# Optimization experiments

Hardware: AMD Instinct MI355X
Metric: run time of the kernel (lower is better)

Reference implementation:

```python
import jax, jax.numpy as jnp
import numpy as np

N_E = 8192
E_DIM = 256
LATENT = 768
OUT_DIM = 768
DECAY = 0.99
EPS = 1e-05
DEAD_THRESH = 0.05
RESET_CS = DEAD_THRESH * 1.2  # reset_cluster_size
RATIO = (8 * 2048) / N_E      # total_codes / n_e with world_size=1


def l2norm(t):
    return t / jnp.linalg.norm(t, axis=-1, keepdims=True)


def setup_inputs() -> dict:
    key = jax.random.key(0)
    ks = jax.random.split(key, 6)
    x = jax.random.normal(ks[0], (8, 2048, LATENT), dtype=jnp.float32)
    # project_in / project_out Linear params (torch Linear: y = x @ W.T + b)
    W_in = jax.random.normal(ks[1], (E_DIM, LATENT), dtype=jnp.float32) * (1.0 / np.sqrt(LATENT))
    b_in = jnp.zeros((E_DIM,), dtype=jnp.float32)
    W_out = jax.random.normal(ks[2], (OUT_DIM, E_DIM), dtype=jnp.float32) * (1.0 / np.sqrt(E_DIM))
    b_out = jnp.zeros((OUT_DIM,), dtype=jnp.float32)
    embed = jax.random.uniform(ks[3], (N_E, E_DIM), dtype=jnp.float32,
                               minval=-1.0 / N_E, maxval=1.0 / N_E)
    embed = l2norm(embed)
    embed_avg = embed
    cluster_size = jnp.ones((N_E,), dtype=jnp.float32) * RATIO  # after init_quantizer
    return {"x": x, "W_in": W_in, "b_in": b_in, "W_out": W_out, "b_out": b_out,
            "embed": embed, "embed_avg": embed_avg, "cluster_size": cluster_size}


def reference(x, W_in, b_in, W_out, b_out, embed, embed_avg, cluster_size):
    sg = jax.lax.stop_gradient
    x_proj = jnp.einsum('btl,el->bte', x, W_in) + b_in        # [B,T,e_dim]
    xf = x_proj.reshape(-1, E_DIM)                            # [n, e_dim]
    xn = l2norm(xf)
    embed_d = sg(embed)
    d = jnp.einsum('nd,cd->nc', xn, embed_d)                  # [n, n_e] similarity
    embed_ind = jnp.argmin(d, axis=1)                         # (faithful: argmin of dot)
    onehot = jax.nn.one_hot(embed_ind, N_E, dtype=jnp.float32)
    z_q = jnp.einsum('nc,cd->nd', onehot, embed_d)            # training path
    bins = onehot.sum(axis=0)                                 # [n_e]
    cluster_new = cluster_size * DECAY + bins * (1.0 - DECAY)
    embed_sum = jnp.einsum('nd,nc->cd', xn, onehot)
    embed_avg_new = embed_avg * DECAY + embed_sum * (1.0 - DECAY)
    # laplace smoothing * total
    total = cluster_new.sum()
    cs = (cluster_new + EPS) / (total + N_E * EPS) * total
    embed_norm = embed_avg_new / cs[:, None]
    # entropy losses on scaled distances
    p = jax.nn.softmax(d * 10.0, axis=-1)                     # [n, n_e]
    ap = p.mean(axis=0)
    entropy_to_max = -(ap * jnp.log(ap)).sum()
    entropy_to_min = (-(p * jnp.log(p)).sum(axis=-1)).mean()
    diversity_loss = -entropy_to_max
    commit_loss = jnp.mean((sg(z_q) - xn) ** 2)
    loss = 1.0 * commit_loss + 1.0 * diversity_loss
    # straight-through estimator
    z_q_st = xn + sg(z_q - xn)
    z_q_out = z_q_st.reshape(x_proj.shape)
    z_q_out = jnp.einsum('bte,oe->bto', z_q_out, W_out) + b_out
    # expire dead codes: replace with first k samples (masked, jit-friendly)
    expired = cluster_new < DEAD_THRESH * RATIO
    n = xn.shape[0]
    idx = jnp.clip(jnp.cumsum(expired.astype(jnp.int32)) - 1, 0, None) % n
    sampled = sg(xn)[idx]                                     # [n_e, e_dim]
    embed_final = jnp.where(expired[:, None], sampled, embed_norm)
    embed_avg_final = jnp.where(expired[:, None], sampled * (RESET_CS * RATIO), embed_avg_new)
    cluster_final = jnp.where(expired, RESET_CS * RATIO, cluster_new)
    return (z_q_out, embed_ind, loss, embed_final, embed_avg_final, cluster_final,
            entropy_to_min, commit_loss)
```

## Files before the change

### kernel.cpp

```cpp
#include <hip/hip_runtime.h>
#include <hip/hip_bf16.h>

typedef unsigned long long u64;
typedef __bf16 bf16_t;
typedef __attribute__((ext_vector_type(8))) __bf16 bf16x8;
typedef __attribute__((ext_vector_type(4))) __bf16 bf16x4;
typedef __attribute__((ext_vector_type(4))) float f32x4;

#define NROWS 16384
#define KLAT  768
#define EDIM  256
#define NE    8192
#define ODIM  768

#define OFF_ZQ   0
#define OFF_IND  12582912
#define OFF_LOSS 12599296
#define OFF_EMB  12599297
#define OFF_EAVG 14696449
#define OFF_CSF  16793601
#define OFF_EMIN 16801793
#define OFF_CMT  16801794

#define W_XN    0u
#define W_ESUM  16777216u
#define W_RMIN  25165824u
#define W_RZ    25296896u
#define W_RS1   25362432u
#define W_INVZ  25427968u
#define W_INDW  25493504u
#define W_BINS  25559040u
#define W_CN    25591808u
#define W_CSM   25624576u
#define W_IDXS  25657344u
#define W_AP    25690112u
#define W_SCAL  25722880u
#define W_END   25722896u

#define CANDCAP 16
#define PROWS   2048
#define PM      128
#define PN      128
#define PK      32

typedef __attribute__((address_space(3))) unsigned char lds_u8;
typedef __attribute__((address_space(1))) const unsigned char glb_u8;
static __device__ __forceinline__ void gload16(const void* g, void* l)
{
  __builtin_amdgcn_global_load_lds((glb_u8*)g, (lds_u8*)l, 16, 0, 0);
}

__global__ __launch_bounds__(256) void zero_out_kernel(float* __restrict__ out, int n)
{
  int i = blockIdx.x * 256 + threadIdx.x;
  if (i < n) out[i] = 0.0f;
}

__global__ __launch_bounds__(256) void gemm_in_kernel(
    const float* __restrict__ A, const float* __restrict__ B,
    const float* __restrict__ bias, float* __restrict__ C)
{
  __shared__ float As[16][64];
  __shared__ float Bs[16][64];
  const int tid = threadIdx.x;
  const int tx = tid & 15, ty = tid >> 4;
  const int bm = blockIdx.x << 6, bn = blockIdx.y << 6;
  const int lr = tid >> 2, lk = (tid & 3) << 2;
  const size_t aoff = (size_t)(bm + lr) * KLAT;
  const size_t boff = (size_t)(bn + lr) * KLAT;
  float acc[4][4] = {};
  for (int k0 = 0; k0 < KLAT; k0 += 16) {
    __syncthreads();
    float4 av = *(const float4*)(A + aoff + k0 + lk);
    float4 bv = *(const float4*)(B + boff + k0 + lk);
    As[lk + 0][lr] = av.x; As[lk + 1][lr] = av.y; As[lk + 2][lr] = av.z; As[lk + 3][lr] = av.w;
    Bs[lk + 0][lr] = bv.x; Bs[lk + 1][lr] = bv.y; Bs[lk + 2][lr] = bv.z; Bs[lk + 3][lr] = bv.w;
    __syncthreads();
#pragma unroll
    for (int kk = 0; kk < 16; ++kk) {
      float4 a4 = *(const float4*)&As[kk][ty << 2];
      float4 b4 = *(const float4*)&Bs[kk][tx << 2];
      float ar[4] = {a4.x, a4.y, a4.z, a4.w};
      float br[4] = {b4.x, b4.y, b4.z, b4.w};
#pragma unroll
      for (int i = 0; i < 4; ++i)
#pragma unroll
        for (int j = 0; j < 4; ++j)
          acc[i][j] = fmaf(ar[i], br[j], acc[i][j]);
    }
  }
  float4 b4 = *(const float4*)(bias + bn + (tx << 2));
  float bb[4] = {b4.x, b4.y, b4.z, b4.w};
#pragma unroll
  for (int i = 0; i < 4; ++i) {
    const size_t row = (size_t)(bm + (ty << 2) + i);
    float4 o = make_float4(acc[i][0] + bb[0], acc[i][1] + bb[1],
                           acc[i][2] + bb[2], acc[i][3] + bb[3]);
    *(float4*)(C + row * EDIM + bn + (tx << 2)) = o;
  }
}

__global__ __launch_bounds__(256) void gemm_out_kernel(
    const float* __restrict__ A, const float* __restrict__ B,
    const float* __restrict__ bias, const int* __restrict__ gather,
    float* __restrict__ C)
{
  __shared__ float As[16][64];
  __shared__ float Bs[16][64];
  const int tid = threadIdx.x;
  const int tx = tid & 15, ty = tid >> 4;
  const int bm = blockIdx.x << 6, bn = blockIdx.y << 6;
  const int lr = tid >> 2, lk = (tid & 3) << 2;
  const size_t arow = (size_t)(gather[bm + lr] & (NE - 1));
  const size_t aoff = arow * EDIM;
  const size_t boff = (size_t)(bn + lr) * EDIM;
  float acc[4][4] = {};
  for (int k0 = 0; k0 < EDIM; k0 += 16) {
    __syncthreads();
    float4 av = *(const float4*)(A + aoff + k0 + lk);
    float4 bv = *(const float4*)(B + boff + k0 + lk);
    As[lk + 0][lr] = av.x; As[lk + 1][lr] = av.y; As[lk + 2][lr] = av.z; As[lk + 3][lr] = av.w;
    Bs[lk + 0][lr] = bv.x; Bs[lk + 1][lr] = bv.y; Bs[lk + 2][lr] = bv.z; Bs[lk + 3][lr] = bv.w;
    __syncthreads();
#pragma unroll
    for (int kk = 0; kk < 16; ++kk) {
      float4 a4 = *(const float4*)&As[kk][ty << 2];
      float4 b4 = *(const float4*)&Bs[kk][tx << 2];
      float ar[4] = {a4.x, a4.y, a4.z, a4.w};
      float br[4] = {b4.x, b4.y, b4.z, b4.w};
#pragma unroll
      for (int i = 0; i < 4; ++i)
#pragma unroll
        for (int j = 0; j < 4; ++j)
          acc[i][j] = fmaf(ar[i], br[j], acc[i][j]);
    }
  }
  float4 b4 = *(const float4*)(bias + bn + (tx << 2));
  float bb[4] = {b4.x, b4.y, b4.z, b4.w};
#pragma unroll
  for (int i = 0; i < 4; ++i) {
    const size_t row = (size_t)(bm + (ty << 2) + i);
    float4 o = make_float4(acc[i][0] + bb[0], acc[i][1] + bb[1],
                           acc[i][2] + bb[2], acc[i][3] + bb[3]);
    *(float4*)(C + row * ODIM + bn + (tx << 2)) = o;
  }
}

__global__ __launch_bounds__(256) void l2norm_split_kernel(
    float* __restrict__ xnf, bf16_t* __restrict__ xh, bf16_t* __restrict__ xl)
{
  __shared__ float sb[4];
  const int r = blockIdx.x, t = threadIdx.x;
  const size_t o = (size_t)r * EDIM + t;
  float v = xnf[o];
  float s = v * v;
#pragma unroll
  for (int off = 32; off >= 1; off >>= 1) s += __shfl_xor(s, off);
  if ((t & 63) == 0) sb[t >> 6] = s;
  __syncthreads();
  float tot = sb[0] + sb[1] + sb[2] + sb[3];
  float nv = v / sqrtf(tot);
  xnf[o] = nv;
  bf16_t h = (bf16_t)nv;
  xh[o] = h;
  xl[o] = (bf16_t)(nv - (float)h);
}

__global__ __launch_bounds__(256) void embed_split_kernel(
    const float* __restrict__ embed, bf16_t* __restrict__ eh, bf16_t* __restrict__ el)
{
  const int i = (blockIdx.x * 256 + threadIdx.x) << 2;
  float4 v = *(const float4*)(embed + i);
  bf16_t h0 = (bf16_t)v.x, h1 = (bf16_t)v.y, h2 = (bf16_t)v.z, h3 = (bf16_t)v.w;
  bf16x4 hv = {h0, h1, h2, h3};
  bf16x4 lv = {(bf16_t)(v.x - (float)h0), (bf16_t)(v.y - (float)h1),
               (bf16_t)(v.z - (float)h2), (bf16_t)(v.w - (float)h3)};
  *(bf16x4*)(eh + i) = hv;
  *(bf16x4*)(el + i) = lv;
}

__global__ __launch_bounds__(256) void phase1_mfma_kernel(
    const bf16_t* __restrict__ xh, const bf16_t* __restrict__ xl,
    const bf16_t* __restrict__ eh, const bf16_t* __restrict__ el,
    const int rowbase,
    u64* __restrict__ rowmin, float* __restrict__ rowZ, float* __restrict__ rowS1,
    bf16_t* __restrict__ P)
{
  __shared__ bf16_t Ab[PM * 64];
  __shared__ bf16_t Bb[PN * 64];
  const int tid  = threadIdx.x;
  const int lane = tid & 63;
  const int wave = tid >> 6;
  const int wm = wave >> 1, wn = wave & 1;
  const int brow = blockIdx.x * PM;
  const int bcol = blockIdx.y * PN;

  const int srow8 = lane >> 3;
  const int chunk = (lane & 7) ^ srow8;
  const bf16_t* gpa = (chunk & 4) ? xl : xh;
  const bf16_t* gpb = (chunk & 4) ? el : eh;
  const int within = (chunk & 3) << 3;
  const int acall0 = wave << 5;

  const bf16_t* ga0 = gpa + (size_t)(rowbase + brow + acall0 + srow8) * EDIM + within;
  const bf16_t* gb0 = gpb + (size_t)(bcol + acall0 + srow8) * EDIM + within;

  f32x4 acc[4][4] = {};

  for (int k0 = 0; k0 < EDIM; k0 += PK) {
    __syncthreads();
#pragma unroll
    for (int c = 0; c < 4; ++c) {
      const int rr = acall0 + (c << 3);
      gload16(ga0 + (size_t)(c << 3) * EDIM + k0, &Ab[rr * 64]);
      gload16(gb0 + (size_t)(c << 3) * EDIM + k0, &Bb[rr * 64]);
    }
    __syncthreads();

    const int swz = lane & 7;
    const int sh  = (lane >> 4) ^ swz;
    const int sl  = sh ^ 4;
    const int ar0 = (wm << 6) + (lane & 15);
    const int br0 = (wn << 6) + (lane & 15);
    bf16x8 bhf[4], blf[4];
#pragma unroll
    for (int n = 0; n < 4; ++n) {
      const int r = br0 + (n << 4);
      bhf[n] = *(const bf16x8*)&Bb[r * 64 + (sh << 3)];
      blf[n] = *(const bf16x8*)&Bb[r * 64 + (sl << 3)];
    }
#pragma unroll
    for (int m = 0; m < 4; ++m) {
      const int r = ar0 + (m << 4);
      bf16x8 ahf = *(const bf16x8*)&Ab[r * 64 + (sh << 3)];
      bf16x8 alf = *(const bf16x8*)&Ab[r * 64 + (sl << 3)];
#pragma unroll
      for (int n = 0; n < 4; ++n) {
        acc[m][n] = __builtin_amdgcn_mfma_f32_16x16x32_bf16(ahf, bhf[n], acc[m][n], 0, 0, 0);
        acc[m][n] = __builtin_amdgcn_mfma_f32_16x16x32_bf16(ahf, blf[n], acc[m][n], 0, 0, 0);
        acc[m][n] = __builtin_amdgcn_mfma_f32_16x16x32_bf16(alf, bhf[n], acc[m][n], 0, 0, 0);
      }
    }
  }

  const int colg  = bcol + (wn << 6) + (lane & 15);
  const int pbase = bcol + (wn << 6) + ((lane & 15) << 2);
  const int rl0   = brow + (wm << 6) + ((lane >> 4) << 2);
#pragma unroll
  for (int m = 0; m < 4; ++m) {
#pragma unroll
    for (int q = 0; q < 4; ++q) {
      const int rl = rl0 + (m << 4) + q;
      float Z = 0.f, S1 = 0.f;
      u64 mk = ~0ull;
      bf16_t evv[4];
#pragma unroll
      for (int n = 0; n < 4; ++n) {
        float d = acc[m][n][q];
        float l = 10.f * d;
        float e = __expf(l);
        Z += e; S1 += l * e;
        evv[n] = (bf16_t)e;
        u64 key = ((u64)__float_as_uint(d + 2.0f) << 32) | (unsigned)(colg + (n << 4));
        if (key < mk) mk = key;
      }
      bf16x4 pv = {evv[0], evv[1], evv[2], evv[3]};
      *(bf16x4*)(P + (size_t)rl * NE + pbase) = pv;
#pragma unroll
      for (int off = 1; off < 16; off <<= 1) {
        u64 ok = __shfl_xor(mk, off);
        if (ok < mk) mk = ok;
        Z  += __shfl_xor(Z, off);
        S1 += __shfl_xor(S1, off);
      }
      if ((lane & 15) == 0) {
        const int rg = rowbase + rl;
        atomicMin(rowmin + rg, mk);
        atomicAdd(rowZ + rg, Z);
        atomicAdd(rowS1 + rg, S1);
      }
    }
  }
}

__global__ __launch_bounds__(256) void colreduce_kernel(
    const bf16_t* __restrict__ P, const float* __restrict__ rowZ,
    const u64* __restrict__ rowmin, const int rowbase,
    float* __restrict__ ap, int* __restrict__ ccnt, int* __restrict__ clist)
{
  __shared__ float izs[64], ths[64];
  const int t = threadIdx.x;
  const int pc0 = blockIdx.x * 1024 + (t << 2);
  const int r0 = blockIdx.y * 64;
  if (t < 64) {
    const int rg = rowbase + r0 + t;
    izs[t] = 1.0f / rowZ[rg];
    float dmin = __uint_as_float((unsigned)(rowmin[rg] >> 32)) - 2.0f;
    ths[t] = __expf(10.f * (dmin + 3e-4f));
  }
  __syncthreads();
  const int Bbase = pc0 & ~63;
  const int sub   = (pc0 & 63) >> 2;
  float s0 = 0.f, s1 = 0.f, s2 = 0.f, s3 = 0.f;
  for (int r = 0; r < 64; ++r) {
    bf16x4 p4 = *(const bf16x4*)(P + (size_t)(r0 + r) * NE + pc0);
    float p0 = (float)p4[0], p1 = (float)p4[1], p2 = (float)p4[2], p3 = (float)p4[3];
    float iz = izs[r], th = ths[r];
    s0 = fmaf(p0, iz, s0); s1 = fmaf(p1, iz, s1);
    s2 = fmaf(p2, iz, s2); s3 = fmaf(p3, iz, s3);
    float pm = fminf(fminf(p0, p1), fminf(p2, p3));
    if (pm <= th) {
      const int rg = rowbase + r0 + r;
      float pvv[4] = {p0, p1, p2, p3};
      for (int n = 0; n < 4; ++n)
        if (pvv[n] <= th) {
          int pos = atomicAdd(ccnt + rg, 1);
          if (pos < CANDCAP) clist[(rg << 4) + pos] = Bbase + (n << 4) + sub;
        }
    }
  }
  atomicAdd(ap + pc0 + 0, s0); atomicAdd(ap + pc0 + 1, s1);
  atomicAdd(ap + pc0 + 2, s2); atomicAdd(ap + pc0 + 3, s3);
}

__global__ __launch_bounds__(256) void rowent_kernel(
    const float* __restrict__ rowZ, const float* __restrict__ rowS1,
    float* __restrict__ scal)
{
  __shared__ float sb[4];
  const int r = blockIdx.x * 256 + threadIdx.x;
  const int t = threadIdx.x;
  float Z = rowZ[r], S1 = rowS1[r];
  float ent = logf(Z) - S1 / Z;
#pragma unroll
  for (int off = 32; off >= 1; off >>= 1) ent += __shfl_xor(ent, off);
  if ((t & 63) == 0) sb[t >> 6] = ent;
  __syncthreads();
  if (t == 0) atomicAdd(scal + 1, sb[0] + sb[1] + sb[2] + sb[3]);
}

__global__ __launch_bounds__(256) void repair_kernel(
    const float* __restrict__ xnf, const float* __restrict__ embed,
    const u64* __restrict__ rowmin, const int* __restrict__ ccnt,
    const int* __restrict__ clist, int* __restrict__ indw,
    float* __restrict__ bins, int* __restrict__ binsI, float* __restrict__ out)
{
  const int t = threadIdx.x;
  const int row = blockIdx.x * 64 + (t >> 2);
  const int sub = t & 3;
  const int base = ((int)(unsigned)(rowmin[row] & 0xFFFFFFFFull)) & (NE - 1);
  int cnt = ccnt[row];
  if (cnt > CANDCAP) cnt = CANDCAP;
  float bestD = 1e30f;
  int bestI = NE;
  const float* xr = xnf + (size_t)row * EDIM + (sub << 6);
  for (int j = -1; j < cnt; ++j) {
    const int c = (j < 0) ? base : (clist[(row << 4) + j] & (NE - 1));
    const float* er = embed + (size_t)c * EDIM + (sub << 6);
    float s = 0.f;
#pragma unroll
    for (int k = 0; k < 64; k += 4) {
      float4 a = *(const float4*)(xr + k);
      float4 b = *(const float4*)(er + k);
      s = fmaf(a.x, b.x, s); s = fmaf(a.y, b.y, s);
      s = fmaf(a.z, b.z, s); s = fmaf(a.w, b.w, s);
    }
    s += __shfl_xor(s, 1);
    s += __shfl_xor(s, 2);
    if (s < bestD || (s == bestD && c < bestI)) { bestD = s; bestI = c; }
  }
  if (sub == 0) {
    indw[row] = bestI;
    out[OFF_IND + row] = (float)bestI;
    atomicAdd(bins + bestI, 1.0f);
    atomicAdd(binsI + bestI, 1);
  }
}

__global__ __launch_bounds__(256) void sortprep_kernel(
    const int* __restrict__ binsI, int* __restrict__ offs, int* __restrict__ cursor)
{
  __shared__ int ssum[256];
  const int t = threadIdx.x;
  const int base = t * 32;
  int loc[32];
  int cnt = 0;
#pragma unroll
  for (int j = 0; j < 32; ++j) { loc[j] = cnt; cnt += binsI[base + j]; }
  ssum[t] = cnt;
  __syncthreads();
  for (int off = 1; off < 256; off <<= 1) {
    int v = (t >= off) ? ssum[t - off] : 0;
    __syncthreads();
    ssum[t] += v;
    __syncthreads();
  }
  int run = (t > 0) ? ssum[t - 1] : 0;
#pragma unroll
  for (int j = 0; j < 32; ++j) {
    offs[base + j]   = run + loc[j];
    cursor[base + j] = run + loc[j];
  }
}

__global__ __launch_bounds__(256) void rowsort_kernel(
    const int* __restrict__ indw, int* __restrict__ cursor, int* __restrict__ sorted)
{
  const int r = blockIdx.x * 256 + threadIdx.x;
  const int ind = indw[r] & (NE - 1);
  int pos = atomicAdd(cursor + ind, 1);
  sorted[pos & (NROWS - 1)] = r;
}

__global__ __launch_bounds__(256) void esum_commit_kernel(
    const int* __restrict__ offs, const int* __restrict__ binsI,
    const int* __restrict__ sorted, const float* __restrict__ xnf,
    const float* __restrict__ embed, float* __restrict__ esum,
    float* __restrict__ scal)
{
  __shared__ float sb[4];
  const int c = blockIdx.x, t = threadIdx.x;
  const float ev = embed[(size_t)c * EDIM + t];
  const int start = offs[c];
  const int cnt = binsI[c];
  float s = 0.f, cm = 0.f;
  for (int j = 0; j < cnt; ++j) {
    const int r = sorted[(start + j) & (NROWS - 1)];
    float xv = xnf[(size_t)r * EDIM + t];
    s += xv;
    float df = ev - xv;
    cm = fmaf(df, df, cm);
  }
  esum[(size_t)c * EDIM + t] = s;
#pragma unroll
  for (int off = 32; off >= 1; off >>= 1) cm += __shfl_xor(cm, off);
  if ((t & 63) == 0) sb[t >> 6] = cm;
  __syncthreads();
  if (t == 0) atomicAdd(scal + 2, sb[0] + sb[1] + sb[2] + sb[3]);
}

__global__ __launch_bounds__(256) void scalars_kernel(
    const float* __restrict__ ap, const float* __restrict__ scal, float* __restrict__ out)
{
  __shared__ float sb[4];
  const int t = threadIdx.x;
  float h = 0.f;
  for (int c = t; c < NE; c += 256) {
    float apv = ap[c] * (1.0f / NROWS);
    h -= apv * logf(apv);
  }
#pragma unroll
  for (int off = 32; off >= 1; off >>= 1) h += __shfl_xor(h, off);
  if ((t & 63) == 0) sb[t >> 6] = h;
  __syncthreads();
  if (t == 0) {
    float Hmax = sb[0] + sb[1] + sb[2] + sb[3];
    float commit = scal[2] * (1.0f / ((float)NROWS * (float)EDIM));
    float emin = scal[1] * (1.0f / (float)NROWS);
    out[OFF_LOSS] = commit - Hmax;
    out[OFF_EMIN] = emin;
    out[OFF_CMT]  = commit;
  }
}

__global__ __launch_bounds__(256) void cluster_kernel(
    const float* __restrict__ cs_in, const float* __restrict__ bins,
    float* __restrict__ cn, float* __restrict__ scal)
{
  __shared__ float sb[4];
  const int c = blockIdx.x * 256 + threadIdx.x;
  const int t = threadIdx.x;
  float v = cs_in[c] * 0.99f + bins[c] * 0.01f;
  cn[c] = v;
  float s = v;
#pragma unroll
  for (int off = 32; off >= 1; off >>= 1) s += __shfl_xor(s, off);
  if ((t & 63) == 0) sb[t >> 6] = s;
  __syncthreads();
  if (t == 0) atomicAdd(scal + 0, sb[0] + sb[1] + sb[2] + sb[3]);
}

__global__ __launch_bounds__(256) void scan_kernel(
    const float* __restrict__ cn, const float* __restrict__ scal,
    int* __restrict__ idxs, float* __restrict__ csm, float* __restrict__ out)
{
  __shared__ int ssum[256];
  const int t = threadIdx.x;
  const int base = t * 32;
  int cnt = 0;
  for (int j = 0; j < 32; ++j) cnt += (cn[base + j] < 0.1f) ? 1 : 0;
  ssum[t] = cnt;
  __syncthreads();
  for (int off = 1; off < 256; off <<= 1) {
    int v = (t >= off) ? ssum[t - off] : 0;
    __syncthreads();
    ssum[t] += v;
    __syncthreads();
  }
  int run = (t > 0) ? ssum[t - 1] : 0;
  const float total = scal[0];
  const float dscale = total / (total + (float)NE * 1e-5f);
  for (int j = 0; j < 32; ++j) {
    float v = cn[base + j];
    bool ex = v < 0.1f;
    run += ex ? 1 : 0;
    int idx = run - 1; if (idx < 0) idx = 0;
    idx &= (NROWS - 1);
    idxs[base + j] = idx;
    csm[base + j] = (v + 1e-5f) * dscale;
    out[OFF_CSF + base + j] = ex ? 0.12f : v;
  }
}

__global__ __launch_bounds__(256) void embed_out_kernel(
    const float* __restrict__ cn, const float* __restrict__ csm,
    const int* __restrict__ idxs, const float* __restrict__ xn,
    const float* __restrict__ embed_avg, const float* __restrict__ esum,
    float* __restrict__ out)
{
  const int c = blockIdx.x, t = threadIdx.x;
  float oe, oa;
  if (cn[c] < 0.1f) {
    float s = xn[(size_t)(idxs[c] & (NROWS - 1)) * EDIM + t];
    oe = s; oa = s * 0.12f;
  } else {
    float an = embed_avg[(size_t)c * EDIM + t] * 0.99f
             + esum[(size_t)c * EDIM + t] * 0.01f;
    oa = an; oe = an / csm[c];
  }
  out[OFF_EMB  + (size_t)c * EDIM + t] = oe;
  out[OFF_EAVG + (size_t)c * EDIM + t] = oa;
}

extern "C" void kernel_launch(void* const* d_in, const int* in_sizes, int n_in,
                              void* d_out, int out_size, void* d_ws, size_t ws_size,
                              hipStream_t stream)
{
  const float* x         = (const float*)d_in[0];
  const float* W_in      = (const float*)d_in[1];
  const float* b_in      = (const float*)d_in[2];
  const float* W_out     = (const float*)d_in[3];
  const float* b_out     = (const float*)d_in[4];
  const float* embed     = (const float*)d_in[5];
  const float* embed_avg = (const float*)d_in[6];
  const float* cs_in     = (const float*)d_in[7];
  float* out = (float*)d_out;
  char* ws = (char*)d_ws;

  if (ws_size < (size_t)W_END) {
    zero_out_kernel<<<(out_size + 255) / 256, 256, 0, stream>>>(out, out_size);
    return;
  }

  bf16_t* xh = (bf16_t*)(ws + W_XN);
  bf16_t* xl = (bf16_t*)(ws + W_XN + 8388608u);
  bf16_t* eh = (bf16_t*)(ws + W_ESUM);
  bf16_t* el = (bf16_t*)(ws + W_ESUM + 4194304u);
  float* esum  = (float*)(ws + W_ESUM);
  u64*   rowmin= (u64*)  (ws + W_RMIN);
  int*   offs  = (int*)  (ws + W_RMIN);
  int*   cursor= offs + NE;
  float* rowZ  = (float*)(ws + W_RZ);
  float* rowS1 = (float*)(ws + W_RS1);
  int*   binsI = (int*)  (ws + W_INVZ);
  int*   indw  = (int*)  (ws + W_INDW);
  float* bins  = (float*)(ws + W_BINS);
  float* cn    = (float*)(ws + W_CN);
  float* csm   = (float*)(ws + W_CSM);
  int*   idxs  = (int*)  (ws + W_IDXS);
  float* ap    = (float*)(ws + W_AP);
  float* scal  = (float*)(ws + W_SCAL);

  float*  xnf    = out + OFF_ZQ;
  bf16_t* Pbuf   = (bf16_t*)(out + OFF_ZQ + 4194304);
  int*    ccnt   = (int*)(out + OFF_EMB);
  int*    clist  = ccnt + NROWS;
  int*    sorted = clist + NROWS * CANDCAP;

  hipMemsetAsync(ws + W_RMIN, 0xFF, W_RZ - W_RMIN, stream);
  hipMemsetAsync(ws + W_RZ,   0,    W_END - W_RZ,  stream);
  hipMemsetAsync(ccnt, 0, NROWS * sizeof(int), stream);

  gemm_in_kernel<<<dim3(NROWS / 64, EDIM / 64), 256, 0, stream>>>(
      x, W_in, b_in, xnf);
  l2norm_split_kernel<<<NROWS, 256, 0, stream>>>(xnf, xh, xl);
  embed_split_kernel<<<(NE * EDIM / 4) / 256, 256, 0, stream>>>(embed, eh, el);
  for (int p = 0; p < NROWS / PROWS; ++p) {
    const int rowbase = p * PROWS;
    phase1_mfma_kernel<<<dim3(PROWS / PM, NE / PN), 256, 0, stream>>>(
        xh, xl, eh, el, rowbase, rowmin, rowZ, rowS1, Pbuf);
    colreduce_kernel<<<dim3(NE / 1024, PROWS / 64), 256, 0, stream>>>(
        Pbuf, rowZ, rowmin, rowbase, ap, ccnt, clist);
  }
  rowent_kernel<<<NROWS / 256, 256, 0, stream>>>(rowZ, rowS1, scal);
  repair_kernel<<<NROWS / 64, 256, 0, stream>>>(
      xnf, embed, rowmin, ccnt, clist, indw, bins, binsI, out);
  sortprep_kernel<<<1, 256, 0, stream>>>(binsI, offs, cursor);
  rowsort_kernel<<<NROWS / 256, 256, 0, stream>>>(indw, cursor, sorted);
  esum_commit_kernel<<<NE, 256, 0, stream>>>(
      offs, binsI, sorted, xnf, embed, esum, scal);
  cluster_kernel<<<NE / 256, 256, 0, stream>>>(cs_in, bins, cn, scal);
  scan_kernel<<<1, 256, 0, stream>>>(cn, scal, idxs, csm, out);
  scalars_kernel<<<1, 256, 0, stream>>>(ap, scal, out);
  embed_out_kernel<<<NE, 256, 0, stream>>>(cn, csm, idxs, xnf, embed_avg, esum, out);
  gemm_out_kernel<<<dim3(NROWS / 64, ODIM / 64), 256, 0, stream>>>(
      embed, W_out, b_out, indw, out + OFF_ZQ);
}
```

Baseline: 1.168 ms.

## Move output projection to split-bf16 MFMA, pad input GEMM LDS, cheapen argmin reduction

Replaces the fp32 SIMT output GEMM with an MFMA kernel. It gathers codebook rows from the bf16 hi/lo split of embed and splits W_out into hi/lo the same way, then uses three MFMAs per tile to keep near-fp32 accuracy. It also pads the input GEMM's shared-memory tiles to reduce LDS bank conflicts. In the phase1 epilogue, the 64-bit key shuffle reduction becomes a float min shuffle, so only lanes holding the minimum issue the atomicMin. Workspace is reshuffled so esum and the W_out split share the old xh/xl region, which relies on those buffers being dead by then.

```diff
diff --git a/kernel.cpp b/kernel.cpp
--- a/kernel.cpp
+++ b/kernel.cpp
@@ -60,8 +60,8 @@
     const float* __restrict__ A, const float* __restrict__ B,
     const float* __restrict__ bias, float* __restrict__ C)
 {
-  __shared__ float As[16][64];
-  __shared__ float Bs[16][64];
+  __shared__ float As[16][68];
+  __shared__ float Bs[16][68];
   const int tid = threadIdx.x;
   const int tx = tid & 15, ty = tid >> 4;
   const int bm = blockIdx.x << 6, bn = blockIdx.y << 6;
@@ -100,52 +100,6 @@
   }
 }
 
-__global__ __launch_bounds__(256) void gemm_out_kernel(
-    const float* __restrict__ A, const float* __restrict__ B,
-    const float* __restrict__ bias, const int* __restrict__ gather,
-    float* __restrict__ C)
-{
-  __shared__ float As[16][64];
-  __shared__ float Bs[16][64];
-  const int tid = threadIdx.x;
-  const int tx = tid & 15, ty = tid >> 4;
-  const int bm = blockIdx.x << 6, bn = blockIdx.y << 6;
-  const int lr = tid >> 2, lk = (tid & 3) << 2;
-  const size_t arow = (size_t)(gather[bm + lr] & (NE - 1));
-  const size_t aoff = arow * EDIM;
-  const size_t boff = (size_t)(bn + lr) * EDIM;
-  float acc[4][4] = {};
-  for (int k0 = 0; k0 < EDIM; k0 += 16) {
-    __syncthreads();
-    float4 av = *(const float4*)(A + aoff + k0 + lk);
-    float4 bv = *(const float4*)(B + boff + k0 + lk);
-    As[lk + 0][lr] = av.x; As[lk + 1][lr] = av.y; As[lk + 2][lr] = av.z; As[lk + 3][lr] = av.w;
-    Bs[lk + 0][lr] = bv.x; Bs[lk + 1][lr] = bv.y; Bs[lk + 2][lr] = bv.z; Bs[lk + 3][lr] = bv.w;
-    __syncthreads();
-#pragma unroll
-    for (int kk = 0; kk < 16; ++kk) {
-      float4 a4 = *(const float4*)&As[kk][ty << 2];
-      float4 b4 = *(const float4*)&Bs[kk][tx << 2];
-      float ar[4] = {a4.x, a4.y, a4.z, a4.w};
-      float br[4] = {b4.x, b4.y, b4.z, b4.w};
-#pragma unroll
-      for (int i = 0; i < 4; ++i)
-#pragma unroll
-        for (int j = 0; j < 4; ++j)
-          acc[i][j] = fmaf(ar[i], br[j], acc[i][j]);
-    }
-  }
-  float4 b4 = *(const float4*)(bias + bn + (tx << 2));
-  float bb[4] = {b4.x, b4.y, b4.z, b4.w};
-#pragma unroll
-  for (int i = 0; i < 4; ++i) {
-    const size_t row = (size_t)(bm + (ty << 2) + i);
-    float4 o = make_float4(acc[i][0] + bb[0], acc[i][1] + bb[1],
-                           acc[i][2] + bb[2], acc[i][3] + bb[3]);
-    *(float4*)(C + row * ODIM + bn + (tx << 2)) = o;
-  }
-}
-
 __global__ __launch_bounds__(256) void l2norm_split_kernel(
     float* __restrict__ xnf, bf16_t* __restrict__ xh, bf16_t* __restrict__ xl)
 {
@@ -166,17 +120,17 @@
   xl[o] = (bf16_t)(nv - (float)h);
 }
 
-__global__ __launch_bounds__(256) void embed_split_kernel(
-    const float* __restrict__ embed, bf16_t* __restrict__ eh, bf16_t* __restrict__ el)
+__global__ __launch_bounds__(256) void split_kernel(
+    const float* __restrict__ src, bf16_t* __restrict__ hi, bf16_t* __restrict__ lo)
 {
   const int i = (blockIdx.x * 256 + threadIdx.x) << 2;
-  float4 v = *(const float4*)(embed + i);
+  float4 v = *(const float4*)(src + i);
   bf16_t h0 = (bf16_t)v.x, h1 = (bf16_t)v.y, h2 = (bf16_t)v.z, h3 = (bf16_t)v.w;
   bf16x4 hv = {h0, h1, h2, h3};
   bf16x4 lv = {(bf16_t)(v.x - (float)h0), (bf16_t)(v.y - (float)h1),
                (bf16_t)(v.z - (float)h2), (bf16_t)(v.w - (float)h3)};
-  *(bf16x4*)(eh + i) = hv;
-  *(bf16x4*)(el + i) = lv;
+  *(bf16x4*)(hi + i) = hv;
+  *(bf16x4*)(lo + i) = lv;
 }
 
 __global__ __launch_bounds__(256) void phase1_mfma_kernel(
@@ -252,7 +206,8 @@
     for (int q = 0; q < 4; ++q) {
       const int rl = rl0 + (m << 4) + q;
       float Z = 0.f, S1 = 0.f;
-      u64 mk = ~0ull;
+      float dloc = 1e30f;
+      int nbest = 0;
       bf16_t evv[4];
 #pragma unroll
       for (int n = 0; n < 4; ++n) {
@@ -261,21 +216,24 @@
         float e = __expf(l);
         Z += e; S1 += l * e;
         evv[n] = (bf16_t)e;
-        u64 key = ((u64)__float_as_uint(d + 2.0f) << 32) | (unsigned)(colg + (n << 4));
-        if (key < mk) mk = key;
+        if (d < dloc) { dloc = d; nbest = n; }
       }
       bf16x4 pv = {evv[0], evv[1], evv[2], evv[3]};
       *(bf16x4*)(P + (size_t)rl * NE + pbase) = pv;
+      float dmin = dloc;
 #pragma unroll
       for (int off = 1; off < 16; off <<= 1) {
-        u64 ok = __shfl_xor(mk, off);
-        if (ok < mk) mk = ok;
+        dmin = fminf(dmin, __shfl_xor(dmin, off));
         Z  += __shfl_xor(Z, off);
         S1 += __shfl_xor(S1, off);
       }
+      const int rg = rowbase + rl;
+      if (dloc == dmin) {
+        u64 key = ((u64)__float_as_uint(dloc + 2.0f) << 32)
+                | (unsigned)(colg + (nbest << 4));
+        atomicMin(rowmin + rg, key);
+      }
       if ((lane & 15) == 0) {
-        const int rg = rowbase + rl;
-        atomicMin(rowmin + rg, mk);
         atomicAdd(rowZ + rg, Z);
         atomicAdd(rowS1 + rg, S1);
       }
@@ -532,6 +490,91 @@
   out[OFF_EAVG + (size_t)c * EDIM + t] = oa;
 }
 
+__global__ __launch_bounds__(256) void gemm_out_mfma_kernel(
+    const bf16_t* __restrict__ eh, const bf16_t* __restrict__ el,
+    const bf16_t* __restrict__ wh, const bf16_t* __restrict__ wl,
+    const float* __restrict__ bias, const int* __restrict__ gather,
+    float* __restrict__ C)
+{
+  __shared__ bf16_t Ab[PM * 64];
+  __shared__ bf16_t Bb[PN * 64];
+  const int tid  = threadIdx.x;
+  const int lane = tid & 63;
+  const int wave = tid >> 6;
+  const int wm = wave >> 1, wn = wave & 1;
+  const int bm   = blockIdx.x * PM;
+  const int bcol = blockIdx.y * PN;
+
+  const int srow8 = lane >> 3;
+  const int chunk = (lane & 7) ^ srow8;
+  const bf16_t* gpa = (chunk & 4) ? el : eh;
+  const bf16_t* gpb = (chunk & 4) ? wl : wh;
+  const int within = (chunk & 3) << 3;
+  const int acall0 = wave << 5;
+
+  const bf16_t* ga[4];
+#pragma unroll
+  for (int c = 0; c < 4; ++c) {
+    const int gr = gather[bm + acall0 + (c << 3) + srow8] & (NE - 1);
+    ga[c] = gpa + (size_t)gr * EDIM + within;
+  }
+  const bf16_t* gb0 = gpb + (size_t)(bcol + acall0 + srow8) * EDIM + within;
+
+  f32x4 acc[4][4] = {};
+
+  for (int k0 = 0; k0 < EDIM; k0 += PK) {
+    __syncthreads();
+#pragma unroll
+    for (int c = 0; c < 4; ++c) {
+      const int rr = acall0 + (c << 3);
+      gload16(ga[c] + k0, &Ab[rr * 64]);
+      gload16(gb0 + (size_t)(c << 3) * EDIM + k0, &Bb[rr * 64]);
+    }
+    __syncthreads();
+
+    const int swz = lane & 7;
+    const int sh  = (lane >> 4) ^ swz;
+    const int sl  = sh ^ 4;
+    const int ar0 = (wm << 6) + (lane & 15);
+    const int br0 = (wn << 6) + (lane & 15);
+    bf16x8 bhf[4], blf[4];
+#pragma unroll
+    for (int n = 0; n < 4; ++n) {
+      const int r = br0 + (n << 4);
+      bhf[n] = *(const bf16x8*)&Bb[r * 64 + (sh << 3)];
+      blf[n] = *(const bf16x8*)&Bb[r * 64 + (sl << 3)];
+    }
+#pragma unroll
+    for (int m = 0; m < 4; ++m) {
+      const int r = ar0 + (m << 4);
+      bf16x8 ahf = *(const bf16x8*)&Ab[r * 64 + (sh << 3)];
+      bf16x8 alf = *(const bf16x8*)&Ab[r * 64 + (sl << 3)];
+#pragma unroll
+      for (int n = 0; n < 4; ++n) {
+        acc[m][n] = __builtin_amdgcn_mfma_f32_16x16x32_bf16(ahf, bhf[n], acc[m][n], 0, 0, 0);
+        acc[m][n] = __builtin_amdgcn_mfma_f32_16x16x32_bf16(ahf, blf[n], acc[m][n], 0, 0, 0);
+        acc[m][n] = __builtin_amdgcn_mfma_f32_16x16x32_bf16(alf, bhf[n], acc[m][n], 0, 0, 0);
+      }
+    }
+  }
+
+  const int colb = bcol + (wn << 6) + (lane & 15);
+  float bs[4];
+#pragma unroll
+  for (int n = 0; n < 4; ++n) bs[n] = bias[colb + (n << 4)];
+  const int row0 = bm + (wm << 6) + ((lane >> 4) << 2);
+#pragma unroll
+  for (int m = 0; m < 4; ++m) {
+#pragma unroll
+    for (int q = 0; q < 4; ++q) {
+      float* op = C + (size_t)(row0 + (m << 4) + q) * ODIM;
+#pragma unroll
+      for (int n = 0; n < 4; ++n)
+        op[colb + (n << 4)] = acc[m][n][q] + bs[n];
+    }
+  }
+}
+
 extern "C" void kernel_launch(void* const* d_in, const int* in_sizes, int n_in,
                               void* d_out, int out_size, void* d_ws, size_t ws_size,
                               hipStream_t stream)
@@ -556,7 +599,9 @@
   bf16_t* xl = (bf16_t*)(ws + W_XN + 8388608u);
   bf16_t* eh = (bf16_t*)(ws + W_ESUM);
   bf16_t* el = (bf16_t*)(ws + W_ESUM + 4194304u);
-  float* esum  = (float*)(ws + W_ESUM);
+  float*  esum = (float*)(ws + W_XN);
+  bf16_t* wh   = (bf16_t*)(ws + W_XN + 8388608u);
+  bf16_t* wl   = (bf16_t*)(ws + W_XN + 8388608u + 393216u);
   u64*   rowmin= (u64*)  (ws + W_RMIN);
   int*   offs  = (int*)  (ws + W_RMIN);
   int*   cursor= offs + NE;
@@ -584,7 +629,7 @@
   gemm_in_kernel<<<dim3(NROWS / 64, EDIM / 64), 256, 0, stream>>>(
       x, W_in, b_in, xnf);
   l2norm_split_kernel<<<NROWS, 256, 0, stream>>>(xnf, xh, xl);
-  embed_split_kernel<<<(NE * EDIM / 4) / 256, 256, 0, stream>>>(embed, eh, el);
+  split_kernel<<<(NE * EDIM / 4) / 256, 256, 0, stream>>>(embed, eh, el);
   for (int p = 0; p < NROWS / PROWS; ++p) {
     const int rowbase = p * PROWS;
     phase1_mfma_kernel<<<dim3(PROWS / PM, NE / PN), 256, 0, stream>>>(
@@ -597,12 +642,13 @@
       xnf, embed, rowmin, ccnt, clist, indw, bins, binsI, out);
   sortprep_kernel<<<1, 256, 0, stream>>>(binsI, offs, cursor);
   rowsort_kernel<<<NROWS / 256, 256, 0, stream>>>(indw, cursor, sorted);
+  split_kernel<<<(ODIM * EDIM / 4) / 256, 256, 0, stream>>>(W_out, wh, wl);
   esum_commit_kernel<<<NE, 256, 0, stream>>>(
       offs, binsI, sorted, xnf, embed, esum, scal);
   cluster_kernel<<<NE / 256, 256, 0, stream>>>(cs_in, bins, cn, scal);
   scan_kernel<<<1, 256, 0, stream>>>(cn, scal, idxs, csm, out);
   scalars_kernel<<<1, 256, 0, stream>>>(ap, scal, out);
   embed_out_kernel<<<NE, 256, 0, stream>>>(cn, csm, idxs, xnf, embed_avg, esum, out);
-  gemm_out_kernel<<<dim3(NROWS / 64, ODIM / 64), 256, 0, stream>>>(
-      embed, W_out, b_out, indw, out + OFF_ZQ);
-}
+  gemm_out_mfma_kernel<<<dim3(NROWS / PM, ODIM / PN), 256, 0, stream>>>(
+      eh, el, wh, wl, b_out, indw, out + OFF_ZQ);
+}
```

After: 1.102 ms. 5.6% less time.
